# Kernel tuning notes

Measured on AMD Instinct MI355X. Metric: run time of the kernel, lower is better.

Reference implementation:

```python
import jax, jax.numpy as jnp
import numpy as np

B, R, C1, C2, C3, K, NC = 512, 200, 32, 32, 512, 8, 2
RATIO = 0.5
K1 = int(np.ceil(RATIO * R))    # 100 nodes kept after pool1
K2 = int(np.ceil(RATIO * K1))   # 50 nodes kept after pool2
EDGE_P = 0.1
NEG = -1e9
BN_EPS = 1e-5
LEAK = 0.01


def setup_inputs() -> dict:
    key = jax.random.key(0)
    ks = jax.random.split(key, 12)

    def lin_w(k, o, i):
        return (jax.random.normal(k, (o, i)) / np.sqrt(i)).astype(jnp.float32)

    return {
        "x": jax.random.normal(ks[0], (B, R, R), dtype=jnp.float32),
        "adj": jax.random.uniform(ks[1], (B, R, R), dtype=jnp.float32),
        "roi": jnp.arange(R, dtype=jnp.int32),
        # conv1 ROI-conditioned weight net: Linear(R->K) -> ReLU -> Linear(K->R*C1)
        "W1a": lin_w(ks[2], K, R), "b1a": jnp.zeros((K,), jnp.float32),
        "W2a": lin_w(ks[3], R * C1, K), "b2a": jnp.zeros((R * C1,), jnp.float32),
        "bias1": jnp.zeros((C1,), jnp.float32),
        # conv2 ROI-conditioned weight net: Linear(R->K) -> ReLU -> Linear(K->C1*C2)
        "W1b": lin_w(ks[4], K, R), "b1b": jnp.zeros((K,), jnp.float32),
        "W2b": lin_w(ks[5], C1 * C2, K), "b2b": jnp.zeros((C1 * C2,), jnp.float32),
        "bias2": jnp.zeros((C2,), jnp.float32),
        # TopK pooling projection vectors
        "wp1": jax.random.normal(ks[6], (C1,), dtype=jnp.float32),
        "wp2": jax.random.normal(ks[7], (C2,), dtype=jnp.float32),
        # MLP head
        "Wm1": lin_w(ks[8], C2, (C1 + C2) * 2), "bm1": jnp.zeros((C2,), jnp.float32),
        "g1": jnp.ones((C2,), jnp.float32), "be1": jnp.zeros((C2,), jnp.float32),
        "Wm2": lin_w(ks[9], C3, C2), "bm2": jnp.zeros((C3,), jnp.float32),
        "g2": jnp.ones((C3,), jnp.float32), "be2": jnp.zeros((C3,), jnp.float32),
        "Ws": lin_w(ks[10], NC, C3), "bs": jnp.zeros((NC,), jnp.float32),
    }


def _nn_table(W1, b1, W2, b2, cin, cout):
    # nn applied to one-hot ROI vectors == table lookup; build the full [R, cin, cout] table once.
    t = jax.nn.relu(W1.T + b1) @ W2.T + b2  # [R, cin*cout]
    return t.reshape(R, cin, cout)


def _gconv(x, w_adj, mask, w_node, bias):
    # per-node ROI-conditioned transform, then edge-softmax weighted aggregation
    if w_node.ndim == 3:   # shared table indexed by arange -> [R,cin,cout]
        xt = jnp.einsum('bni,nio->bno', x, w_node)
    else:                   # gathered per graph -> [B,n,cin,cout]
        xt = jnp.einsum('bni,bnio->bno', x, w_node)
    n = x.shape[1]
    eye = jnp.eye(n, dtype=bool)
    # remove self loops, add self loop with weight 1, softmax over incoming edges
    logits = jnp.where(mask & ~eye, w_adj, NEG)
    logits = jnp.where(eye, 1.0, logits)
    att = jax.nn.softmax(logits, axis=-1)  # row i = incoming edges of node i
    return jnp.einsum('bij,bjo->bio', att, xt) + bias


def _topk_pool(h, w_adj, mask, roi, w, k):
    s = jax.nn.sigmoid(h @ w / jnp.linalg.norm(w))  # [B, n]
    vals, perm = jax.lax.top_k(s, k)
    xs = jnp.take_along_axis(h, perm[:, :, None], axis=1) * vals[:, :, None]
    b = jnp.arange(h.shape[0])[:, None, None]
    w_sub = w_adj[b, perm[:, :, None], perm[:, None, :]]
    m_sub = mask[b, perm[:, :, None], perm[:, None, :]]
    roi_sub = roi[perm] if roi.ndim == 1 else jnp.take_along_axis(roi, perm, axis=1)
    return xs, w_sub, m_sub, roi_sub, vals


def _augment(w_adj, mask):
    # add_self_loops(fill=1) -> spspmm(A, A) -> remove_self_loops, in dense-batched form
    n = w_adj.shape[1]
    eye = jnp.eye(n, dtype=bool)
    wd = jnp.where(mask & ~eye, w_adj, 0.0)
    wd = jnp.where(eye, 1.0, wd)
    a2 = jnp.einsum('bij,bjk->bik', wd, wd)
    m2 = (a2 != 0.0) & ~eye
    a2 = jnp.where(eye, 0.0, a2)
    return a2, m2


def _mlp_block(y, Wl, bl, g, be):
    y = y @ Wl.T + bl
    y = jnp.where(y > 0, y, LEAK * y)          # LeakyReLU(0.01)
    mu = jnp.mean(y, axis=0)
    var = jnp.var(y, axis=0)                    # training-mode BatchNorm1d
    return g * (y - mu) * jax.lax.rsqrt(var + BN_EPS) + be


def _forward(x, adj, roi, W1a, b1a, W2a, b2a, bias1, W1b, b1b, W2b, b2b, bias2,
             wp1, wp2, Wm1, bm1, g1, be1, Wm2, bm2, g2, be2, Ws, bs):
    mask0 = adj < EDGE_P
    wtab1 = _nn_table(W1a, b1a, W2a, b2a, R, C1)   # [R, R, C1]
    h1 = _gconv(x, adj, mask0, wtab1[roi], bias1)  # [B, R, C1]
    x1, w1, m1, roi1, vals1 = _topk_pool(h1, adj, mask0, roi, wp1, K1)
    a_aug, m_aug = _augment(w1, m1)                 # 2-hop augmented adjacency
    wtab2 = _nn_table(W1b, b1b, W2b, b2b, C1, C2)  # [R, C1, C2]
    h2 = _gconv(x1, a_aug, m_aug, wtab2[roi1], bias2)  # [B, K1, C2]
    x2, _, _, _, vals2 = _topk_pool(h2, a_aug, m_aug, roi1, wp2, K2)
    # readout: [gmp, gap] per level, concatenated -> (C1+C2)*2 = 128
    feat = jnp.concatenate([x1.max(1), x1.mean(1), x2.max(1), x2.mean(1)], axis=-1)
    y = _mlp_block(feat, Wm1, bm1, g1, be1)
    y = _mlp_block(y, Wm2, bm2, g2, be2)
    logp = jax.nn.log_softmax(y @ Ws.T + bs, axis=-1)
    return logp, jax.nn.sigmoid(vals1), jax.nn.sigmoid(vals2)


def reference(x, adj, roi, W1a, b1a, W2a, b2a, bias1, W1b, b1b, W2b, b2b, bias2,
              wp1, wp2, Wm1, bm1, g1, be1, Wm2, bm2, g2, be2, Ws, bs):
    logp, s1, s2 = _forward(x, adj, roi, W1a, b1a, W2a, b2a, bias1,
                            W1b, b1b, W2b, b2b, bias2, wp1, wp2,
                            Wm1, bm1, g1, be1, Wm2, bm2, g2, be2, Ws, bs)
    return (logp, wp1, wp2, s1, s2)
```

## Files before the change

kernel.cpp:

```cpp
#include <hip/hip_runtime.h>
#include <math.h>

#define NB 512
#define RR 200
#define KK1 100
#define KK2 50

__device__ __forceinline__ float sigm(float v) { return 1.0f / (1.0f + expf(-v)); }

__global__ void k_tab(const float* __restrict__ W1, const float* __restrict__ b1,
                      const float* __restrict__ W2, const float* __restrict__ b2,
                      float* __restrict__ tab, int OUT) {
  int n = blockIdx.x;
  __shared__ float h[8];
  if (threadIdx.x < 8) {
    float v = W1[threadIdx.x * RR + n] + b1[threadIdx.x];
    h[threadIdx.x] = v > 0.f ? v : 0.f;
  }
  __syncthreads();
  for (int j = threadIdx.x; j < OUT; j += 256) {
    float acc = b2[j];
#pragma unroll
    for (int k = 0; k < 8; k++) acc += h[k] * W2[j * 8 + k];
    tab[(size_t)n * OUT + j] = acc;
  }
}

__global__ void k_norm(const float* __restrict__ wp1, const float* __restrict__ wp2,
                       float* __restrict__ norms) {
  int t = threadIdx.x;
  float a = (t < 32) ? wp1[t] * wp1[t] : 0.f;
  float b = (t < 32) ? wp2[t] * wp2[t] : 0.f;
  for (int s = 32; s; s >>= 1) { a += __shfl_xor(a, s); b += __shfl_xor(b, s); }
  if (t == 0) { norms[0] = sqrtf(a); norms[1] = sqrtf(b); }
}

__global__ __launch_bounds__(128) void k_xt1(const float* __restrict__ x,
                                             const float* __restrict__ wtab1,
                                             float* __restrict__ xt1) {
  int n = blockIdx.x, t = threadIdx.x;
  __shared__ float wsm[6400];
  for (int idx = t; idx < 1600; idx += 128)
    *(float4*)&wsm[idx * 4] = *(const float4*)(wtab1 + (size_t)n * 6400 + idx * 4);
  __syncthreads();
  int bg = t >> 3, og = t & 7;
  int b0 = blockIdx.y * 64 + bg * 4;
  const float* xp = x + (size_t)b0 * 40000 + (size_t)n * 200;
  float acc[4][4] = {};
  float4 A[4], Bf[4], N0[4] = {}, N1[4] = {};
#pragma unroll
  for (int r = 0; r < 4; r++) A[r] = *(const float4*)(xp + (size_t)r * 40000);
#pragma unroll
  for (int r = 0; r < 4; r++) Bf[r] = *(const float4*)(xp + (size_t)r * 40000 + 4);
  for (int g = 0; g < 50; g += 2) {
    int i = g * 4;
    if (g + 2 < 50) {
#pragma unroll
      for (int r = 0; r < 4; r++) N0[r] = *(const float4*)(xp + (size_t)r * 40000 + i + 8);
#pragma unroll
      for (int r = 0; r < 4; r++) N1[r] = *(const float4*)(xp + (size_t)r * 40000 + i + 12);
    }
#pragma unroll
    for (int k = 0; k < 4; k++) {
      float4 w4 = *(const float4*)&wsm[(i + k) * 32 + og * 4];
#pragma unroll
      for (int r = 0; r < 4; r++) {
        float xs = (&A[r].x)[k];
        acc[r][0] += xs * w4.x; acc[r][1] += xs * w4.y;
        acc[r][2] += xs * w4.z; acc[r][3] += xs * w4.w;
      }
    }
#pragma unroll
    for (int k = 0; k < 4; k++) {
      float4 w4 = *(const float4*)&wsm[(i + 4 + k) * 32 + og * 4];
#pragma unroll
      for (int r = 0; r < 4; r++) {
        float xs = (&Bf[r].x)[k];
        acc[r][0] += xs * w4.x; acc[r][1] += xs * w4.y;
        acc[r][2] += xs * w4.z; acc[r][3] += xs * w4.w;
      }
    }
#pragma unroll
    for (int r = 0; r < 4; r++) { A[r] = N0[r]; Bf[r] = N1[r]; }
  }
#pragma unroll
  for (int r = 0; r < 4; r++)
    *(float4*)(xt1 + (size_t)(b0 + r) * 6400 + (size_t)n * 32 + og * 4) =
        make_float4(acc[r][0], acc[r][1], acc[r][2], acc[r][3]);
}

__global__ __launch_bounds__(1024) void k_att1(const float* __restrict__ adj,
                                               const float* __restrict__ xt1,
                                               const float* __restrict__ bias1,
                                               const float* __restrict__ wp1,
                                               const float* __restrict__ norms,
                                               float* __restrict__ h1, float* __restrict__ sc1) {
  int t = threadIdx.x;
  __shared__ float2 pvj[16][4][56];
  int w = t >> 6, lane = t & 63;
  int og = lane & 7, jp = lane >> 3;
  float4 bias4 = *(const float4*)(bias1 + og * 4);
  float4 wp4 = *(const float4*)(wp1 + og * 4);
  float nrm = norms[0];
  unsigned long long ltmask = (1ull << lane) - 1ull;
  int npass = (w < 2) ? 4 : 3;
  int total = 2 * npass;
  float av[4][4];
  {
    int b0 = blockIdx.x * 2;
    int r00 = w * 4;
    const float* abase = adj + (size_t)b0 * 40000 + (size_t)r00 * 200;
#pragma unroll
    for (int r = 0; r < 4; r++)
#pragma unroll
      for (int s2 = 0; s2 < 4; s2++) {
        int j = lane + 64 * s2;
        av[r][s2] = (j < RR) ? __builtin_nontemporal_load(abase + r * 200 + j) : 1.0f;
      }
  }
  for (int idx = 0; idx < total; idx++) {
    int second = (idx >= npass) ? 1 : 0;
    int b = blockIdx.x * 2 + second;
    int pass = idx - second * npass;
    int r0 = pass * 64 + w * 4;
    float ls[4];
    int cnt[4];
#pragma unroll
    for (int r = 0; r < 4; r++) {
      int i = r0 + r;
      float e[4];
      bool nz[4];
#pragma unroll
      for (int s2 = 0; s2 < 4; s2++) {
        int j = lane + 64 * s2;
        float a = av[r][s2];
        bool keep = (j < RR) && ((j == i) || (a < 0.1f));
        float lg = (j == i) ? 1.0f : a;
        e[s2] = keep ? __expf(lg - 1.0f) : 0.f;
        nz[s2] = keep;
      }
      float lsum = e[0] + e[1] + e[2] + e[3];
      int base = 0;
#pragma unroll
      for (int s2 = 0; s2 < 4; s2++) {
        unsigned long long m = __ballot(nz[s2]);
        if (nz[s2]) pvj[w][r][base + __popcll(m & ltmask)] = make_float2(e[s2], (float)(lane + 64 * s2));
        base += __popcll(m);
      }
      cnt[r] = base;
      for (int s = 32; s; s >>= 1) lsum += __shfl_xor(lsum, s);
      ls[r] = lsum;
    }
    if (idx + 1 < total) {
      int idx2 = idx + 1;
      int sec2 = (idx2 >= npass) ? 1 : 0;
      int b2 = blockIdx.x * 2 + sec2;
      int r02 = (idx2 - sec2 * npass) * 64 + w * 4;
      const float* abase = adj + (size_t)b2 * 40000 + (size_t)r02 * 200;
#pragma unroll
      for (int r = 0; r < 4; r++)
#pragma unroll
        for (int s2 = 0; s2 < 4; s2++) {
          int j = lane + 64 * s2;
          if (j < RR) av[r][s2] = __builtin_nontemporal_load(abase + r * 200 + j);
        }
    }
    const float* xtb = xt1 + (size_t)b * 6400 + og * 4;
    float acc[4][4] = {};
#pragma unroll
    for (int r = 0; r < 4; r++) {
      for (int q = jp; q < cnt[r]; q += 8) {
        float2 pe = pvj[w][r][q];
        int jj = (int)pe.y;
        float4 xv = *(const float4*)(xtb + jj * 32);
        acc[r][0] += pe.x * xv.x; acc[r][1] += pe.x * xv.y;
        acc[r][2] += pe.x * xv.z; acc[r][3] += pe.x * xv.w;
      }
    }
#pragma unroll
    for (int r = 0; r < 4; r++) {
#pragma unroll
      for (int c = 0; c < 4; c++) {
        float v = acc[r][c];
        v += __shfl_xor(v, 8); v += __shfl_xor(v, 16); v += __shfl_xor(v, 32);
        acc[r][c] = v;
      }
    }
#pragma unroll
    for (int r = 0; r < 4; r++) {
      if (jp == r) {
        float inv = 1.0f / ls[r];
        float4 h4 = make_float4(acc[r][0] * inv + bias4.x, acc[r][1] * inv + bias4.y,
                                acc[r][2] * inv + bias4.z, acc[r][3] * inv + bias4.w);
        *(float4*)(h1 + ((size_t)b * RR + r0 + r) * 32 + og * 4) = h4;
        float tt = h4.x * wp4.x + h4.y * wp4.y + h4.z * wp4.z + h4.w * wp4.w;
        tt += __shfl_xor(tt, 1); tt += __shfl_xor(tt, 2); tt += __shfl_xor(tt, 4);
        if (og == 0) sc1[b * RR + r0 + r] = sigm(tt / nrm);
      }
    }
  }
}

__global__ void k_top1(const float* __restrict__ sc1, int* __restrict__ perm1,
                       float* __restrict__ vals1, float* __restrict__ out_s1) {
  int b = blockIdx.x, t = threadIdx.x;
  __shared__ float s[RR];
  for (int i = t; i < RR; i += 256) s[i] = sc1[b * RR + i];
  __syncthreads();
  for (int i = t; i < RR; i += 256) {
    float si = s[i];
    int rank = 0;
    for (int j = 0; j < RR; j++) {
      float sj = s[j];
      rank += (sj > si) || (sj == si && j < i);
    }
    if (rank < KK1) {
      perm1[b * KK1 + rank] = i;
      vals1[b * KK1 + rank] = si;
      out_s1[b * KK1 + rank] = sigm(si);
    }
  }
}

__global__ __launch_bounds__(256) void k_stage2a(const float* __restrict__ h1,
                                                 const float* __restrict__ wtab2,
                                                 const int* __restrict__ perm1,
                                                 const float* __restrict__ vals1,
                                                 float* __restrict__ xt2,
                                                 float* __restrict__ feat) {
  int b = blockIdx.x, t = threadIdx.x;
  int kbase = blockIdx.y * 50;
  __shared__ float x1s[KK1 * 33];
  __shared__ int pk[KK1];
  __shared__ float vk[KK1];
  if (t < KK1) { pk[t] = perm1[b * KK1 + t]; vk[t] = vals1[b * KK1 + t]; }
  __syncthreads();
  for (int i = t; i < KK1 * 32; i += 256) {
    int k = i >> 5, o = i & 31;
    x1s[k * 33 + o] = h1[((size_t)b * RR + pk[k]) * 32 + o] * vk[k];
  }
  __syncthreads();
  if (blockIdx.y == 0 && t < 32) {
    float mx = -3e38f, sm = 0.f;
    for (int k = 0; k < KK1; k++) { float v = x1s[k * 33 + t]; mx = fmaxf(mx, v); sm += v; }
    feat[b * 128 + t] = mx;
    feat[b * 128 + 32 + t] = sm / 100.0f;
  }
  int w = t >> 6, lane = t & 63;
  int og = lane & 7, kq = lane >> 3;
#pragma unroll
  for (int pass = 0; pass < 2; pass++) {
    int kl = pass * 32 + w * 8 + kq;
    if (kl < 50) {
      int kg = kbase + kl;
      const float* W = wtab2 + (size_t)pk[kg] * 1024 + og * 4;
      float4 a4 = make_float4(0.f, 0.f, 0.f, 0.f);
#pragma unroll 8
      for (int ii = 0; ii < 32; ii++) {
        float4 w4 = *(const float4*)(W + ii * 32);
        float xs = x1s[kg * 33 + ii];
        a4.x += xs * w4.x; a4.y += xs * w4.y; a4.z += xs * w4.z; a4.w += xs * w4.w;
      }
      *(float4*)(xt2 + (size_t)b * 3200 + kg * 32 + og * 4) = a4;
    }
  }
}

__global__ __launch_bounds__(256) void k_wd(const float* __restrict__ adj,
                                            const int* __restrict__ perm1,
                                            float* __restrict__ wd) {
  int b = blockIdx.x, t = threadIdx.x;
  int g0 = blockIdx.y * 20;
  __shared__ float rowbuf[20][200];
  __shared__ int pk[KK1];
  if (t < KK1) pk[t] = perm1[b * KK1 + t];
  __syncthreads();
  for (int idx = t; idx < 4000; idx += 256) {
    int r = idx / 200, j = idx - r * 200;
    rowbuf[r][j] = adj[(size_t)b * 40000 + (size_t)pk[g0 + r] * 200 + j];
  }
  __syncthreads();
  for (int idx = t; idx < 2000; idx += 256) {
    int r = idx / 100, k2 = idx - r * 100;
    int k1 = g0 + r;
    float v;
    if (k1 == k2) v = 1.0f;
    else {
      float av = rowbuf[r][pk[k2]];
      v = (av < 0.1f) ? av : 0.0f;
    }
    wd[(size_t)b * (KK1 * KK1) + k1 * KK1 + k2] = v;
  }
}

__global__ __launch_bounds__(512) void k_stage2b(const float* __restrict__ wd,
                                                 const float* __restrict__ xt2,
                                                 const float* __restrict__ bias2,
                                                 const float* __restrict__ wp2,
                                                 const float* __restrict__ norms,
                                                 float* __restrict__ h2, float* __restrict__ sc2) {
  int b = blockIdx.x, t = threadIdx.x;
  __shared__ float wds[KK1][100];
  __shared__ float xts[KK1 * 32];
  __shared__ float pT[8][KK1][4];
  __shared__ int   nzidx[KK1][36];
  int w = t >> 6, lane = t & 63;
  unsigned long long ltmask = (1ull << lane) - 1ull;
  float bias_o = bias2[lane & 31];
  float wp_o = wp2[lane & 31];
  float nrm = norms[1];
  int k2a = lane;
  int k2b = lane + 64;
  bool vb = k2b < KK1;
  for (int i = t; i < KK1 * KK1; i += 512) ((float*)wds)[i] = wd[(size_t)b * (KK1 * KK1) + i];
  for (int idx = t; idx < 800; idx += 512)
    *(float4*)&xts[idx * 4] = *(const float4*)(xt2 + (size_t)b * 3200 + idx * 4);
  __syncthreads();
  for (int r = w; r < KK1; r += 8) {
    bool nz0 = (wds[r][lane] != 0.f);
    bool nz1 = (lane < KK1 - 64) && (wds[r][64 + lane] != 0.f);
    unsigned long long m0 = __ballot(nz0);
    unsigned long long m1 = __ballot(nz1);
    int c0 = __popcll(m0);
    int cnt = c0 + __popcll(m1);
    if (nz0) nzidx[r][__popcll(m0 & ltmask)] = lane;
    if (nz1) nzidx[r][c0 + __popcll(m1 & ltmask)] = 64 + lane;
    int pad = (4 - (cnt & 3)) & 3;
    if (lane < pad) nzidx[r][cnt + lane] = 0;
    if (lane == 0) nzidx[r][35] = cnt;
  }
  __syncthreads();
  for (int g = w; g < 25; g += 8) {
    int r0 = g * 4;
    float acc[4][2];
#pragma unroll
    for (int r = 0; r < 4; r++) {
      int k1 = r0 + r;
      int cnt = nzidx[k1][35];
      float s0 = 0.f, s1 = 0.f;
      for (int it = 0; it < cnt; it += 4) {
        int4 m4 = *(const int4*)&nzidx[k1][it];
        float a0 = wds[k1][m4.x];
        float a1 = (it + 1 < cnt) ? wds[k1][m4.y] : 0.f;
        float a2v = (it + 2 < cnt) ? wds[k1][m4.z] : 0.f;
        float a3 = (it + 3 < cnt) ? wds[k1][m4.w] : 0.f;
        s0 += a0 * wds[m4.x][k2a]; s1 += a0 * wds[m4.x][k2b];
        s0 += a1 * wds[m4.y][k2a]; s1 += a1 * wds[m4.y][k2b];
        s0 += a2v * wds[m4.z][k2a]; s1 += a2v * wds[m4.z][k2b];
        s0 += a3 * wds[m4.w][k2a]; s1 += a3 * wds[m4.w][k2b];
      }
      acc[r][0] = s0; acc[r][1] = s1;
    }
    float p0[4], p1[4], rs[4];
#pragma unroll
    for (int r = 0; r < 4; r++) {
      int k1 = r0 + r;
      float lv0 = (k1 == k2a) ? 1.0f : ((acc[r][0] != 0.0f) ? acc[r][0] : -1e9f);
      float lv1 = (k1 == k2b) ? 1.0f : ((acc[r][1] != 0.0f) ? acc[r][1] : -1e9f);
      float mx = vb ? fmaxf(lv0, lv1) : lv0;
      for (int s = 32; s; s >>= 1) mx = fmaxf(mx, __shfl_xor(mx, s));
      float e0 = expf(lv0 - mx);
      float e1 = vb ? expf(lv1 - mx) : 0.f;
      float ls = e0 + e1;
      for (int s = 32; s; s >>= 1) ls += __shfl_xor(ls, s);
      p0[r] = e0; p1[r] = e1; rs[r] = 1.0f / ls;
    }
    *(float4*)&pT[w][k2a][0] = make_float4(p0[0] * rs[0], p0[1] * rs[1], p0[2] * rs[2], p0[3] * rs[3]);
    if (vb) *(float4*)&pT[w][k2b][0] = make_float4(p1[0] * rs[0], p1[1] * rs[1], p1[2] * rs[2], p1[3] * rs[3]);
    int half = lane >> 5, o = lane & 31;
    float hv[4] = {0.f, 0.f, 0.f, 0.f};
    for (int jj = 0; jj < 50; jj++) {
      int j = half * 50 + jj;
      float4 pv = *(const float4*)&pT[w][j][0];
      float xv = xts[j * 32 + o];
      hv[0] += pv.x * xv; hv[1] += pv.y * xv; hv[2] += pv.z * xv; hv[3] += pv.w * xv;
    }
#pragma unroll
    for (int r = 0; r < 4; r++) hv[r] += __shfl_down(hv[r], 32);
    if (lane < 32) {
#pragma unroll
      for (int r = 0; r < 4; r++) {
        float h = hv[r] + bias_o;
        h2[((size_t)b * KK1 + (r0 + r)) * 32 + o] = h;
        float tt = h * wp_o;
        for (int s = 16; s; s >>= 1) tt += __shfl_xor(tt, s);
        if (lane == 0) sc2[b * KK1 + (r0 + r)] = sigm(tt / nrm);
      }
    }
  }
}

__global__ void k_feat2(const float* __restrict__ sc2, const float* __restrict__ h2,
                        float* __restrict__ out_s2, float* __restrict__ feat) {
  int b = blockIdx.x, t = threadIdx.x;
  __shared__ float s[KK1];
  __shared__ int p2[KK2];
  __shared__ float v2[KK2];
  for (int i = t; i < KK1; i += 256) s[i] = sc2[b * KK1 + i];
  __syncthreads();
  for (int i = t; i < KK1; i += 256) {
    float si = s[i];
    int rank = 0;
    for (int j = 0; j < KK1; j++) {
      float sj = s[j];
      rank += (sj > si) || (sj == si && j < i);
    }
    if (rank < KK2) {
      p2[rank] = i;
      v2[rank] = si;
      out_s2[b * KK2 + rank] = sigm(si);
    }
  }
  __syncthreads();
  if (t < 32) {
    float mx = -3e38f, sm = 0.f;
    for (int k = 0; k < KK2; k++) {
      float v = h2[((size_t)b * KK1 + p2[k]) * 32 + t] * v2[k];
      mx = fmaxf(mx, v);
      sm += v;
    }
    feat[b * 128 + 64 + t] = mx;
    feat[b * 128 + 96 + t] = sm / 50.0f;
  }
}

__global__ void k_mlp1(const float* __restrict__ feat, const float* __restrict__ Wm1,
                       const float* __restrict__ bm1, float* __restrict__ y1) {
  __shared__ float Wt[128 * 32];
  __shared__ float f[8][128];
  int t = threadIdx.x;
  for (int i = t; i < 4096; i += 256) { int c = i >> 7, d = i & 127; Wt[d * 32 + c] = Wm1[i]; }
  int b0 = blockIdx.x * 8;
  for (int i = t; i < 1024; i += 256) f[i >> 7][i & 127] = feat[b0 * 128 + i];
  __syncthreads();
  int bl = t >> 5, c = t & 31;
  float acc = bm1[c];
#pragma unroll 4
  for (int d = 0; d < 128; d++) acc += f[bl][d] * Wt[d * 32 + c];
  y1[(b0 + bl) * 32 + c] = acc > 0.f ? acc : 0.01f * acc;
}

__global__ void k_bn(const float* __restrict__ y, int C, float* __restrict__ stats) {
  int c = blockIdx.x, t = threadIdx.x;
  __shared__ float ys[512];
  __shared__ float red[8];
  ys[t] = y[(size_t)t * C + c];
  ys[t + 256] = y[(size_t)(t + 256) * C + c];
  __syncthreads();
  float s = ys[t] + ys[t + 256];
  for (int d = 32; d; d >>= 1) s += __shfl_xor(s, d);
  if ((t & 63) == 0) red[t >> 6] = s;
  __syncthreads();
  float mu = (red[0] + red[1] + red[2] + red[3]) * (1.0f / 512.0f);
  float d0 = ys[t] - mu, d1 = ys[t + 256] - mu;
  float v = d0 * d0 + d1 * d1;
  for (int d = 32; d; d >>= 1) v += __shfl_xor(v, d);
  if ((t & 63) == 0) red[4 + (t >> 6)] = v;
  __syncthreads();
  if (t == 0) {
    float var = (red[4] + red[5] + red[6] + red[7]) * (1.0f / 512.0f);
    stats[c] = mu;
    stats[C + c] = rsqrtf(var + 1e-5f);
  }
}

__global__ void k_mlp2(const float* __restrict__ y1, const float* __restrict__ st1,
                       const float* __restrict__ g1, const float* __restrict__ be1,
                       const float* __restrict__ Wm2, const float* __restrict__ bm2,
                       float* __restrict__ y2) {
  __shared__ float yn[32];
  int b = blockIdx.x, t = threadIdx.x;
  if (t < 32) {
    float v = y1[b * 32 + t];
    yn[t] = g1[t] * (v - st1[t]) * st1[32 + t] + be1[t];
  }
  __syncthreads();
  for (int c = t; c < 512; c += 256) {
    float acc = bm2[c];
#pragma unroll
    for (int k = 0; k < 32; k++) acc += yn[k] * Wm2[c * 32 + k];
    y2[(size_t)b * 512 + c] = acc > 0.f ? acc : 0.01f * acc;
  }
}

__global__ void k_final(const float* __restrict__ y2, const float* __restrict__ st2,
                        const float* __restrict__ g2, const float* __restrict__ be2,
                        const float* __restrict__ Ws, const float* __restrict__ bs,
                        float* __restrict__ out) {
  int w = threadIdx.x >> 6, lane = threadIdx.x & 63;
  int b = blockIdx.x * 4 + w;
  float z0 = 0.f, z1 = 0.f;
  for (int c = lane; c < 512; c += 64) {
    float v = g2[c] * (y2[(size_t)b * 512 + c] - st2[c]) * st2[512 + c] + be2[c];
    z0 += v * Ws[c];
    z1 += v * Ws[512 + c];
  }
  for (int s = 32; s; s >>= 1) { z0 += __shfl_xor(z0, s); z1 += __shfl_xor(z1, s); }
  if (lane == 0) {
    z0 += bs[0];
    z1 += bs[1];
    float m = fmaxf(z0, z1);
    float lse = m + logf(expf(z0 - m) + expf(z1 - m));
    out[b * 2] = z0 - lse;
    out[b * 2 + 1] = z1 - lse;
  }
}

__global__ void k_copy(const float* __restrict__ wp1, const float* __restrict__ wp2,
                       float* __restrict__ out) {
  int t = threadIdx.x;
  if (t < 32) out[1024 + t] = wp1[t];
  else if (t < 64) out[1056 + (t - 32)] = wp2[t - 32];
}

extern "C" void kernel_launch(void* const* d_in, const int* in_sizes, int n_in,
                              void* d_out, int out_size, void* d_ws, size_t ws_size,
                              hipStream_t stream) {
  const float* x    = (const float*)d_in[0];
  const float* adj  = (const float*)d_in[1];
  const float* W1a  = (const float*)d_in[3];
  const float* b1a  = (const float*)d_in[4];
  const float* W2a  = (const float*)d_in[5];
  const float* b2a  = (const float*)d_in[6];
  const float* bias1= (const float*)d_in[7];
  const float* W1b  = (const float*)d_in[8];
  const float* b1b  = (const float*)d_in[9];
  const float* W2b  = (const float*)d_in[10];
  const float* b2b  = (const float*)d_in[11];
  const float* bias2= (const float*)d_in[12];
  const float* wp1  = (const float*)d_in[13];
  const float* wp2  = (const float*)d_in[14];
  const float* Wm1  = (const float*)d_in[15];
  const float* bm1  = (const float*)d_in[16];
  const float* g1   = (const float*)d_in[17];
  const float* be1  = (const float*)d_in[18];
  const float* Wm2  = (const float*)d_in[19];
  const float* bm2  = (const float*)d_in[20];
  const float* g2   = (const float*)d_in[21];
  const float* be2  = (const float*)d_in[22];
  const float* Ws   = (const float*)d_in[23];
  const float* bs   = (const float*)d_in[24];
  float* out = (float*)d_out;

  float* ws = (float*)d_ws;
  float* WTAB1 = ws;
  float* WTAB2 = WTAB1 + 1280000;
  float* NORMS = WTAB2 + 204800;
  float* XT1   = NORMS + 16;
  float* H1    = XT1 + 3276800;
  float* SC1   = H1 + 3276800;
  float* VALS1 = SC1 + 102400;
  int*   PERM1 = (int*)(VALS1 + 51200);
  float* XT2   = (float*)(PERM1 + 51200);
  float* WD    = XT2 + 1638400;
  float* H2    = WD + 5120000;
  float* SC2   = H2 + 1638400;
  float* FEAT  = SC2 + 51200;
  float* Y1    = FEAT + 65536;
  float* ST1   = Y1 + 16384;
  float* Y2    = ST1 + 64;
  float* ST2   = Y2 + 262144;

  k_tab<<<200, 256, 0, stream>>>(W1a, b1a, W2a, b2a, WTAB1, 6400);
  k_tab<<<200, 256, 0, stream>>>(W1b, b1b, W2b, b2b, WTAB2, 1024);
  k_norm<<<1, 64, 0, stream>>>(wp1, wp2, NORMS);
  k_xt1<<<dim3(200, 8), 128, 0, stream>>>(x, WTAB1, XT1);
  k_att1<<<256, 1024, 0, stream>>>(adj, XT1, bias1, wp1, NORMS, H1, SC1);
  k_top1<<<512, 256, 0, stream>>>(SC1, PERM1, VALS1, out + 1088);
  k_stage2a<<<dim3(512, 2), 256, 0, stream>>>(H1, WTAB2, PERM1, VALS1, XT2, FEAT);
  k_wd<<<dim3(512, 5), 256, 0, stream>>>(adj, PERM1, WD);
  k_stage2b<<<512, 512, 0, stream>>>(WD, XT2, bias2, wp2, NORMS, H2, SC2);
  k_feat2<<<512, 256, 0, stream>>>(SC2, H2, out + 52288, FEAT);
  k_mlp1<<<64, 256, 0, stream>>>(FEAT, Wm1, bm1, Y1);
  k_bn<<<32, 256, 0, stream>>>(Y1, 32, ST1);
  k_mlp2<<<512, 256, 0, stream>>>(Y1, ST1, g1, be1, Wm2, bm2, Y2);
  k_bn<<<512, 256, 0, stream>>>(Y2, 512, ST2);
  k_final<<<128, 256, 0, stream>>>(Y2, ST2, g2, be2, Ws, bs, out);
  k_copy<<<1, 64, 0, stream>>>(wp1, wp2, out);
}
```

Measured before the change: 224.1 us.

## Restructure k_att1 so each 8-lane group aggregates one row serially

Each wave now handles 8 adjacency rows per pass instead of 4. The neighbor aggregation is remapped so each 8-lane group owns one full row and walks its compacted neighbor list serially, instead of splitting each row across 8 groups. This removes the cross-lane shuffle reductions and the separate softmax-sum reduction, which is now folded into the aggregation loop. In exchange each group runs a longer serial loop, per-row counts go through shared memory, and the adj prefetch doubles the register footprint.

```diff
diff --git a/kernel.cpp b/kernel.cpp
--- a/kernel.cpp
+++ b/kernel.cpp
@@ -96,22 +96,21 @@
                                                const float* __restrict__ norms,
                                                float* __restrict__ h1, float* __restrict__ sc1) {
   int t = threadIdx.x;
-  __shared__ float2 pvj[16][4][56];
+  __shared__ float2 pvj[16][8][49];
+  __shared__ int cntS[16][8];
   int w = t >> 6, lane = t & 63;
-  int og = lane & 7, jp = lane >> 3;
+  int rq = lane >> 3, og = lane & 7;
   float4 bias4 = *(const float4*)(bias1 + og * 4);
   float4 wp4 = *(const float4*)(wp1 + og * 4);
   float nrm = norms[0];
   unsigned long long ltmask = (1ull << lane) - 1ull;
-  int npass = (w < 2) ? 4 : 3;
+  int npass = (w < 9) ? 2 : 1;
   int total = 2 * npass;
-  float av[4][4];
+  float av[8][4];
   {
-    int b0 = blockIdx.x * 2;
-    int r00 = w * 4;
-    const float* abase = adj + (size_t)b0 * 40000 + (size_t)r00 * 200;
-#pragma unroll
-    for (int r = 0; r < 4; r++)
+    const float* abase = adj + (size_t)(blockIdx.x * 2) * 40000 + (size_t)(w * 8) * 200;
+#pragma unroll
+    for (int r = 0; r < 8; r++)
 #pragma unroll
       for (int s2 = 0; s2 < 4; s2++) {
         int j = lane + 64 * s2;
@@ -122,11 +121,9 @@
     int second = (idx >= npass) ? 1 : 0;
     int b = blockIdx.x * 2 + second;
     int pass = idx - second * npass;
-    int r0 = pass * 64 + w * 4;
-    float ls[4];
-    int cnt[4];
-#pragma unroll
-    for (int r = 0; r < 4; r++) {
+    int r0 = pass * 128 + w * 8;
+#pragma unroll
+    for (int r = 0; r < 8; r++) {
       int i = r0 + r;
       float e[4];
       bool nz[4];
@@ -139,7 +136,6 @@
         e[s2] = keep ? __expf(lg - 1.0f) : 0.f;
         nz[s2] = keep;
       }
-      float lsum = e[0] + e[1] + e[2] + e[3];
       int base = 0;
 #pragma unroll
       for (int s2 = 0; s2 < 4; s2++) {
@@ -147,57 +143,40 @@
         if (nz[s2]) pvj[w][r][base + __popcll(m & ltmask)] = make_float2(e[s2], (float)(lane + 64 * s2));
         base += __popcll(m);
       }
-      cnt[r] = base;
-      for (int s = 32; s; s >>= 1) lsum += __shfl_xor(lsum, s);
-      ls[r] = lsum;
+      if (lane == 0) cntS[w][r] = base;
     }
     if (idx + 1 < total) {
       int idx2 = idx + 1;
       int sec2 = (idx2 >= npass) ? 1 : 0;
       int b2 = blockIdx.x * 2 + sec2;
-      int r02 = (idx2 - sec2 * npass) * 64 + w * 4;
+      int r02 = (idx2 - sec2 * npass) * 128 + w * 8;
       const float* abase = adj + (size_t)b2 * 40000 + (size_t)r02 * 200;
 #pragma unroll
-      for (int r = 0; r < 4; r++)
+      for (int r = 0; r < 8; r++)
 #pragma unroll
         for (int s2 = 0; s2 < 4; s2++) {
           int j = lane + 64 * s2;
           if (j < RR) av[r][s2] = __builtin_nontemporal_load(abase + r * 200 + j);
         }
     }
+    int cnt = cntS[w][rq];
     const float* xtb = xt1 + (size_t)b * 6400 + og * 4;
-    float acc[4][4] = {};
-#pragma unroll
-    for (int r = 0; r < 4; r++) {
-      for (int q = jp; q < cnt[r]; q += 8) {
-        float2 pe = pvj[w][r][q];
-        int jj = (int)pe.y;
-        float4 xv = *(const float4*)(xtb + jj * 32);
-        acc[r][0] += pe.x * xv.x; acc[r][1] += pe.x * xv.y;
-        acc[r][2] += pe.x * xv.z; acc[r][3] += pe.x * xv.w;
-      }
-    }
-#pragma unroll
-    for (int r = 0; r < 4; r++) {
-#pragma unroll
-      for (int c = 0; c < 4; c++) {
-        float v = acc[r][c];
-        v += __shfl_xor(v, 8); v += __shfl_xor(v, 16); v += __shfl_xor(v, 32);
-        acc[r][c] = v;
-      }
-    }
-#pragma unroll
-    for (int r = 0; r < 4; r++) {
-      if (jp == r) {
-        float inv = 1.0f / ls[r];
-        float4 h4 = make_float4(acc[r][0] * inv + bias4.x, acc[r][1] * inv + bias4.y,
-                                acc[r][2] * inv + bias4.z, acc[r][3] * inv + bias4.w);
-        *(float4*)(h1 + ((size_t)b * RR + r0 + r) * 32 + og * 4) = h4;
-        float tt = h4.x * wp4.x + h4.y * wp4.y + h4.z * wp4.z + h4.w * wp4.w;
-        tt += __shfl_xor(tt, 1); tt += __shfl_xor(tt, 2); tt += __shfl_xor(tt, 4);
-        if (og == 0) sc1[b * RR + r0 + r] = sigm(tt / nrm);
-      }
-    }
+    float a0 = 0.f, a1 = 0.f, a2 = 0.f, a3 = 0.f, lsum = 0.f;
+    for (int q = 0; q < cnt; q++) {
+      float2 pe = pvj[w][rq][q];
+      int jj = (int)pe.y;
+      float4 xv = *(const float4*)(xtb + jj * 32);
+      lsum += pe.x;
+      a0 += pe.x * xv.x; a1 += pe.x * xv.y; a2 += pe.x * xv.z; a3 += pe.x * xv.w;
+    }
+    float inv = 1.0f / lsum;
+    int i = r0 + rq;
+    float4 h4 = make_float4(a0 * inv + bias4.x, a1 * inv + bias4.y,
+                            a2 * inv + bias4.z, a3 * inv + bias4.w);
+    *(float4*)(h1 + ((size_t)b * RR + i) * 32 + og * 4) = h4;
+    float tt = h4.x * wp4.x + h4.y * wp4.y + h4.z * wp4.z + h4.w * wp4.w;
+    tt += __shfl_xor(tt, 1); tt += __shfl_xor(tt, 2); tt += __shfl_xor(tt, 4);
+    if (og == 0) sc1[b * RR + i] = sigm(tt / nrm);
   }
 }
 
```

Result: faster. 210.3 us (-6.1%).
